# Optimization experiments

Measured on AMD Instinct MI355X. Metric: run time of the kernel, lower is better.

The kernel has to match this reference:

```python
import jax, jax.numpy as jnp
import numpy as np

N_NODES = 100000
N_EDGES = 1600000
IN_DIM = 64
OUT_DIM = 64
BN_EPS = 1e-5


def batchnorm(h, gamma, beta):
    # BatchNorm1d in training mode: per-feature batch stats, biased variance
    mean = jnp.mean(h, axis=0)
    var = jnp.mean((h - mean) ** 2, axis=0)
    return gamma * (h - mean) * jax.lax.rsqrt(var + BN_EPS) + beta


def setup_inputs() -> dict:
    key = jax.random.key(0)
    ks = jax.random.split(key, 4)
    x = jax.random.normal(ks[0], (N_NODES, IN_DIM), dtype=jnp.float32)
    edge_index = jax.random.randint(ks[1], (2, N_EDGES), 0, N_NODES, dtype=jnp.int32)
    epsilon = jnp.asarray(0.1, dtype=jnp.float32)
    # Linear weights stored [in, out] (transpose of torch layout)
    W1 = jax.random.normal(ks[2], (IN_DIM, 2 * OUT_DIM), dtype=jnp.float32) * (1.0 / np.sqrt(IN_DIM))
    b1 = jnp.zeros((2 * OUT_DIM,), dtype=jnp.float32)
    g1 = jnp.ones((2 * OUT_DIM,), dtype=jnp.float32)
    be1 = jnp.zeros((2 * OUT_DIM,), dtype=jnp.float32)
    W2 = jax.random.normal(ks[3], (2 * OUT_DIM, OUT_DIM), dtype=jnp.float32) * (1.0 / np.sqrt(2 * OUT_DIM))
    b2 = jnp.zeros((OUT_DIM,), dtype=jnp.float32)
    g2 = jnp.ones((OUT_DIM,), dtype=jnp.float32)
    be2 = jnp.zeros((OUT_DIM,), dtype=jnp.float32)
    return {"x": x, "edge_index": edge_index, "epsilon": epsilon,
            "W1": W1, "b1": b1, "g1": g1, "be1": be1,
            "W2": W2, "b2": b2, "g2": g2, "be2": be2}


def reference(x, edge_index, epsilon, W1, b1, g1, be1, W2, b2, g2, be2):
    src, dst = edge_index[0], edge_index[1]
    # gather messages from src, scatter-add into dst  [N, D]
    neighbor_sum = jnp.zeros_like(x).at[dst].add(x[src])
    combined = (1.0 + epsilon) * x + neighbor_sum
    h = combined @ W1 + b1            # [N, 2*out_dim]
    h = jax.nn.relu(batchnorm(h, g1, be1))
    h = h @ W2 + b2                   # [N, out_dim]
    return batchnorm(h, g2, be2)
```

## Files before the change

kernel.cpp:

```cpp
#include <hip/hip_runtime.h>

#define N_NODES 100000
#define N_EDGES 1600000
#define IN_DIM 64
#define H_DIM 128
#define OUT_DIM 64
#define BN_EPS 1e-5f
#define CAP 64
#define BIN_SHIFT 9
#define BIN_NODES 512
#define NB 256
#define NBIN_BLOCKS ((N_NODES + BIN_NODES - 1) / BIN_NODES)

#define OFF_XB    0
#define OFF_COMB  3200000
#define OFF_H1    6400000
#define OFF_H2    12800000
#define OFF_STATS 19200000
#define S1SUM 0
#define S1SQ  128
#define S2SUM 256
#define S2SQ  320
#define STATS_FLOATS 768

#define DEV_ATOMIC_ADD(p, v) __hip_atomic_fetch_add((p), (v), __ATOMIC_RELAXED, __HIP_MEMORY_SCOPE_AGENT)

typedef __attribute__((ext_vector_type(8))) short short8;
typedef __attribute__((ext_vector_type(4))) float f32x4;

__device__ __forceinline__ unsigned short f2bf(float f) {
  union { float f; unsigned u; } v; v.f = f;
  unsigned r = v.u + 0x7FFFu + ((v.u >> 16) & 1u);
  return (unsigned short)(r >> 16);
}
__device__ __forceinline__ float bflo(unsigned v) { union { unsigned u; float f; } t; t.u = v << 16; return t.f; }
__device__ __forceinline__ float bfhi(unsigned v) { union { unsigned u; float f; } t; t.u = v & 0xFFFF0000u; return t.f; }

__device__ __forceinline__ void acc8(float* a, uint4 v) {
  a[0] += bflo(v.x); a[1] += bfhi(v.x); a[2] += bflo(v.y); a[3] += bfhi(v.y);
  a[4] += bflo(v.z); a[5] += bfhi(v.z); a[6] += bflo(v.w); a[7] += bfhi(v.w);
}
__device__ __forceinline__ uint4 pack8(const float* a) {
  uint4 o;
  o.x = (unsigned)f2bf(a[0]) | ((unsigned)f2bf(a[1]) << 16);
  o.y = (unsigned)f2bf(a[2]) | ((unsigned)f2bf(a[3]) << 16);
  o.z = (unsigned)f2bf(a[4]) | ((unsigned)f2bf(a[5]) << 16);
  o.w = (unsigned)f2bf(a[6]) | ((unsigned)f2bf(a[7]) << 16);
  return o;
}

__global__ __launch_bounds__(256) void k_cvt(const float* __restrict__ x,
                                             unsigned short* __restrict__ xb) {
  int i = blockIdx.x * 256 + threadIdx.x;
  if (i < N_NODES * IN_DIM / 4) {
    float4 v = ((const float4*)x)[i];
    ushort4 o;
    o.x = f2bf(v.x); o.y = f2bf(v.y); o.z = f2bf(v.z); o.w = f2bf(v.w);
    *(ushort4*)(xb + i * 4) = o;
  }
}

__global__ __launch_bounds__(256) void k_bhist(const int* __restrict__ ei,
                                               int* __restrict__ bhist) {
  __shared__ int h[NB];
  const int tid = threadIdx.x;
  h[tid] = 0;
  __syncthreads();
  #pragma unroll
  for (int j = 0; j < 8; ++j) {
    int e = blockIdx.x * 2048 + j * 256 + tid;
    if (e < N_EDGES) atomicAdd(&h[ei[N_EDGES + e] >> BIN_SHIFT], 1);
  }
  __syncthreads();
  if (h[tid]) DEV_ATOMIC_ADD(&bhist[tid], h[tid]);
}

__global__ __launch_bounds__(256) void k_scan256(const int* __restrict__ bhist,
                                                 int* __restrict__ boff,
                                                 int* __restrict__ bcur) {
  __shared__ int s[NB];
  const int tid = threadIdx.x;
  int v = bhist[tid];
  s[tid] = v;
  __syncthreads();
  for (int d = 1; d < NB; d <<= 1) {
    int t = (tid >= d) ? s[tid - d] : 0;
    __syncthreads();
    s[tid] += t;
    __syncthreads();
  }
  int incl = s[tid];
  boff[tid] = incl - v;
  if (tid == NB - 1) boff[NB] = incl;
  bcur[tid] = incl - v;
}

__global__ __launch_bounds__(256) void k_bsplit(const int* __restrict__ ei,
                                                int* __restrict__ bcur,
                                                int2* __restrict__ binned) {
  __shared__ int lcnt[NB];
  __shared__ int lofs[NB];
  __shared__ int lbase[NB];
  __shared__ int sc[NB];
  __shared__ int2 staged[2048];
  const int tid = threadIdx.x;
  lcnt[tid] = 0;
  __syncthreads();
  int src[8], dst[8], rk[8];
  #pragma unroll
  for (int j = 0; j < 8; ++j) {
    int e = blockIdx.x * 2048 + j * 256 + tid;
    if (e < N_EDGES) {
      src[j] = ei[e];
      dst[j] = ei[N_EDGES + e];
      rk[j] = atomicAdd(&lcnt[dst[j] >> BIN_SHIFT], 1);
    } else {
      src[j] = -1;
    }
  }
  __syncthreads();
  int v = lcnt[tid];
  sc[tid] = v;
  __syncthreads();
  for (int d = 1; d < NB; d <<= 1) {
    int t = (tid >= d) ? sc[tid - d] : 0;
    __syncthreads();
    sc[tid] += t;
    __syncthreads();
  }
  lofs[tid] = sc[tid] - v;
  if (v > 0) lbase[tid] = DEV_ATOMIC_ADD(&bcur[tid], v);
  __syncthreads();
  #pragma unroll
  for (int j = 0; j < 8; ++j) {
    if (src[j] >= 0) {
      int b = dst[j] >> BIN_SHIFT;
      staged[lofs[b] + rk[j]] = make_int2(src[j], dst[j]);
    }
  }
  int nv = sc[NB - 1];
  __syncthreads();
  for (int i = tid; i < nv; i += 256) {
    int2 e = staged[i];
    int b = e.y >> BIN_SHIFT;
    binned[lbase[b] + (i - lofs[b])] = e;
  }
}

__global__ __launch_bounds__(512) void k_bfill(const int* __restrict__ boff,
                                               const int2* __restrict__ binned,
                                               int* __restrict__ cnt,
                                               int* __restrict__ srcl) {
  __shared__ int lcnt[BIN_NODES];
  const int tid = threadIdx.x;
  for (int i = tid; i < BIN_NODES; i += 512) lcnt[i] = 0;
  __syncthreads();
  const int b = blockIdx.x;
  const int s = boff[b], e = boff[b + 1];
  const int base = b * BIN_NODES;
  for (int i = s + tid; i < e; i += 512) {
    int2 ed = binned[i];
    int pos = atomicAdd(&lcnt[ed.y - base], 1);
    if (pos < CAP) srcl[ed.y * CAP + pos] = ed.x;
  }
  __syncthreads();
  for (int i = tid; i < BIN_NODES; i += 512) {
    int node = base + i;
    if (node < N_NODES) cnt[node] = lcnt[i];
  }
}

__global__ __launch_bounds__(256) void k_gather(const unsigned short* __restrict__ xb,
                                                const float* __restrict__ eps,
                                                const int* __restrict__ cnt,
                                                const int* __restrict__ srcl,
                                                unsigned short* __restrict__ comb) {
  int gid = blockIdx.x * 256 + threadIdx.x;
  int node = gid >> 2;
  int c = gid & 3;
  if (node >= N_NODES) return;
  float a[16];
  #pragma unroll
  for (int i = 0; i < 16; ++i) a[i] = 0.f;
  const unsigned short* bp = xb + node * 64 + c * 16;
  acc8(a, *(const uint4*)bp);
  acc8(a + 8, *(const uint4*)(bp + 8));
  float e = 1.0f + eps[0];
  #pragma unroll
  for (int i = 0; i < 16; ++i) a[i] *= e;
  int deg = cnt[node];
  if (deg > CAP) deg = CAP;
  const int* sl = srcl + node * CAP;
  int j = 0;
  for (; j + 2 <= deg; j += 2) {
    int s0 = sl[j], s1 = sl[j + 1];
    const unsigned short* p0 = xb + s0 * 64 + c * 16;
    const unsigned short* p1 = xb + s1 * 64 + c * 16;
    uint4 v0 = *(const uint4*)p0;
    uint4 v1 = *(const uint4*)(p0 + 8);
    uint4 w0 = *(const uint4*)p1;
    uint4 w1 = *(const uint4*)(p1 + 8);
    acc8(a, v0); acc8(a + 8, v1);
    acc8(a, w0); acc8(a + 8, w1);
  }
  if (j < deg) {
    const unsigned short* p0 = xb + sl[j] * 64 + c * 16;
    acc8(a, *(const uint4*)p0);
    acc8(a + 8, *(const uint4*)(p0 + 8));
  }
  unsigned short* op = comb + node * 64 + c * 16;
  *(uint4*)op = pack8(a);
  *(uint4*)(op + 8) = pack8(a + 8);
}

#define APAD 72
__global__ __launch_bounds__(256) void k_gemm1(const unsigned short* __restrict__ comb,
                                               const float* __restrict__ W1,
                                               const float* __restrict__ b1,
                                               unsigned short* __restrict__ h1,
                                               float* __restrict__ stats) {
  __shared__ unsigned short As[128 * APAD];
  __shared__ unsigned short Ws[128 * APAD];
  __shared__ float red[4][128];
  const int tid = threadIdx.x;
  const int wv = tid >> 6, lane = tid & 63;
  const int quad = lane >> 4, ln = lane & 15;
  const int rowBase = blockIdx.x * 128;

  #pragma unroll
  for (int it = 0; it < 4; ++it) {
    int idx = it * 256 + tid;
    int row = idx >> 3, ch = idx & 7;
    int gRow = rowBase + row;
    uint4 v = (gRow < N_NODES) ? *(const uint4*)(comb + gRow * 64 + ch * 8)
                               : make_uint4(0, 0, 0, 0);
    *(uint4*)&As[row * APAD + ch * 8] = v;
  }
  #pragma unroll
  for (int it = 0; it < 8; ++it) {
    int idx = it * 256 + tid;
    int k = idx >> 5, n4 = idx & 31;
    float4 wv1 = *(const float4*)(W1 + k * 128 + n4 * 4);
    Ws[(n4 * 4 + 0) * APAD + k] = f2bf(wv1.x);
    Ws[(n4 * 4 + 1) * APAD + k] = f2bf(wv1.y);
    Ws[(n4 * 4 + 2) * APAD + k] = f2bf(wv1.z);
    Ws[(n4 * 4 + 3) * APAD + k] = f2bf(wv1.w);
  }
  __syncthreads();

  f32x4 acc[2][8];
  #pragma unroll
  for (int mt = 0; mt < 2; ++mt) {
    #pragma unroll
    for (int nt = 0; nt < 8; ++nt) acc[mt][nt] = (f32x4)0.0f;
  }
  const int rw = wv * 32;
  #pragma unroll
  for (int kb = 0; kb < 2; ++kb) {
    short8 a0 = *(short8*)&As[(rw + ln) * APAD + kb * 32 + quad * 8];
    short8 a1 = *(short8*)&As[(rw + 16 + ln) * APAD + kb * 32 + quad * 8];
    #pragma unroll
    for (int nt = 0; nt < 8; ++nt) {
      short8 b = *(short8*)&Ws[(nt * 16 + ln) * APAD + kb * 32 + quad * 8];
      acc[0][nt] = __builtin_amdgcn_mfma_f32_16x16x32_bf16(a0, b, acc[0][nt], 0, 0, 0);
      acc[1][nt] = __builtin_amdgcn_mfma_f32_16x16x32_bf16(a1, b, acc[1][nt], 0, 0, 0);
    }
  }

  float bias[8], s[8], q[8];
  #pragma unroll
  for (int nt = 0; nt < 8; ++nt) { bias[nt] = b1[nt * 16 + ln]; s[nt] = 0.f; q[nt] = 0.f; }
  #pragma unroll
  for (int mt = 0; mt < 2; ++mt) {
    #pragma unroll
    for (int i = 0; i < 4; ++i) {
      int gRow = rowBase + rw + mt * 16 + quad * 4 + i;
      if (gRow < N_NODES) {
        #pragma unroll
        for (int nt = 0; nt < 8; ++nt) {
          float v = acc[mt][nt][i] + bias[nt];
          h1[gRow * 128 + nt * 16 + ln] = f2bf(v);
          s[nt] += v; q[nt] += v * v;
        }
      }
    }
  }
  #pragma unroll
  for (int nt = 0; nt < 8; ++nt) {
    s[nt] += __shfl_xor(s[nt], 16); s[nt] += __shfl_xor(s[nt], 32);
    q[nt] += __shfl_xor(q[nt], 16); q[nt] += __shfl_xor(q[nt], 32);
  }
  if (lane < 16) {
    #pragma unroll
    for (int nt = 0; nt < 8; ++nt) red[wv][nt * 16 + ln] = s[nt];
  }
  __syncthreads();
  if (tid < 128) DEV_ATOMIC_ADD(&stats[S1SUM + tid],
                                red[0][tid] + red[1][tid] + red[2][tid] + red[3][tid]);
  __syncthreads();
  if (lane < 16) {
    #pragma unroll
    for (int nt = 0; nt < 8; ++nt) red[wv][nt * 16 + ln] = q[nt];
  }
  __syncthreads();
  if (tid < 128) DEV_ATOMIC_ADD(&stats[S1SQ + tid],
                                red[0][tid] + red[1][tid] + red[2][tid] + red[3][tid]);
}

#define WPAD 136
__global__ __launch_bounds__(256) void k_gemm2(const unsigned short* __restrict__ h1,
                                               const float* __restrict__ W2,
                                               const float* __restrict__ b2,
                                               const float* __restrict__ g1,
                                               const float* __restrict__ be1,
                                               unsigned short* __restrict__ h2,
                                               float* __restrict__ stats) {
  __shared__ unsigned short As[128 * APAD];
  __shared__ unsigned short Ws[64 * WPAD];
  __shared__ float red[4][64];
  __shared__ float scL[128], shL[128];
  const int tid = threadIdx.x;
  const int wv = tid >> 6, lane = tid & 63;
  const int quad = lane >> 4, ln = lane & 15;
  const int rowBase = blockIdx.x * 128;

  if (tid < 128) {
    float mean = stats[S1SUM + tid] * (1.0f / N_NODES);
    float var = stats[S1SQ + tid] * (1.0f / N_NODES) - mean * mean;
    var = fmaxf(var, 0.0f);
    float sc = g1[tid] * rsqrtf(var + BN_EPS);
    scL[tid] = sc;
    shL[tid] = be1[tid] - mean * sc;
  }
  #pragma unroll
  for (int it = 0; it < 8; ++it) {
    int idx = it * 256 + tid;
    int k = idx >> 4, n4 = idx & 15;
    float4 wv2 = *(const float4*)(W2 + k * 64 + n4 * 4);
    Ws[(n4 * 4 + 0) * WPAD + k] = f2bf(wv2.x);
    Ws[(n4 * 4 + 1) * WPAD + k] = f2bf(wv2.y);
    Ws[(n4 * 4 + 2) * WPAD + k] = f2bf(wv2.z);
    Ws[(n4 * 4 + 3) * WPAD + k] = f2bf(wv2.w);
  }

  f32x4 acc[2][4];
  #pragma unroll
  for (int mt = 0; mt < 2; ++mt) {
    #pragma unroll
    for (int nt = 0; nt < 4; ++nt) acc[mt][nt] = (f32x4)0.0f;
  }
  const int rw = wv * 32;

  for (int kc = 0; kc < 2; ++kc) {
    __syncthreads();
    #pragma unroll
    for (int it = 0; it < 4; ++it) {
      int idx = it * 256 + tid;
      int row = idx >> 3, ch = idx & 7;
      int gRow = rowBase + row;
      uint4 u = (gRow < N_NODES) ? *(const uint4*)(h1 + gRow * 128 + kc * 64 + ch * 8)
                                 : make_uint4(0, 0, 0, 0);
      int kb = kc * 64 + ch * 8;
      float f0 = fmaxf(bflo(u.x) * scL[kb + 0] + shL[kb + 0], 0.f);
      float f1 = fmaxf(bfhi(u.x) * scL[kb + 1] + shL[kb + 1], 0.f);
      float f2 = fmaxf(bflo(u.y) * scL[kb + 2] + shL[kb + 2], 0.f);
      float f3 = fmaxf(bfhi(u.y) * scL[kb + 3] + shL[kb + 3], 0.f);
      float f4 = fmaxf(bflo(u.z) * scL[kb + 4] + shL[kb + 4], 0.f);
      float f5 = fmaxf(bfhi(u.z) * scL[kb + 5] + shL[kb + 5], 0.f);
      float f6 = fmaxf(bflo(u.w) * scL[kb + 6] + shL[kb + 6], 0.f);
      float f7 = fmaxf(bfhi(u.w) * scL[kb + 7] + shL[kb + 7], 0.f);
      uint4 o;
      o.x = (unsigned)f2bf(f0) | ((unsigned)f2bf(f1) << 16);
      o.y = (unsigned)f2bf(f2) | ((unsigned)f2bf(f3) << 16);
      o.z = (unsigned)f2bf(f4) | ((unsigned)f2bf(f5) << 16);
      o.w = (unsigned)f2bf(f6) | ((unsigned)f2bf(f7) << 16);
      *(uint4*)&As[row * APAD + ch * 8] = o;
    }
    __syncthreads();
    #pragma unroll
    for (int kb = 0; kb < 2; ++kb) {
      short8 a0 = *(short8*)&As[(rw + ln) * APAD + kb * 32 + quad * 8];
      short8 a1 = *(short8*)&As[(rw + 16 + ln) * APAD + kb * 32 + quad * 8];
      #pragma unroll
      for (int nt = 0; nt < 4; ++nt) {
        short8 b = *(short8*)&Ws[(nt * 16 + ln) * WPAD + kc * 64 + kb * 32 + quad * 8];
        acc[0][nt] = __builtin_amdgcn_mfma_f32_16x16x32_bf16(a0, b, acc[0][nt], 0, 0, 0);
        acc[1][nt] = __builtin_amdgcn_mfma_f32_16x16x32_bf16(a1, b, acc[1][nt], 0, 0, 0);
      }
    }
  }

  float bias[4], s[4], q[4];
  #pragma unroll
  for (int nt = 0; nt < 4; ++nt) { bias[nt] = b2[nt * 16 + ln]; s[nt] = 0.f; q[nt] = 0.f; }
  #pragma unroll
  for (int mt = 0; mt < 2; ++mt) {
    #pragma unroll
    for (int i = 0; i < 4; ++i) {
      int gRow = rowBase + rw + mt * 16 + quad * 4 + i;
      if (gRow < N_NODES) {
        #pragma unroll
        for (int nt = 0; nt < 4; ++nt) {
          float v = acc[mt][nt][i] + bias[nt];
          h2[gRow * 64 + nt * 16 + ln] = f2bf(v);
          s[nt] += v; q[nt] += v * v;
        }
      }
    }
  }
  #pragma unroll
  for (int nt = 0; nt < 4; ++nt) {
    s[nt] += __shfl_xor(s[nt], 16); s[nt] += __shfl_xor(s[nt], 32);
    q[nt] += __shfl_xor(q[nt], 16); q[nt] += __shfl_xor(q[nt], 32);
  }
  if (lane < 16) {
    #pragma unroll
    for (int nt = 0; nt < 4; ++nt) red[wv][nt * 16 + ln] = s[nt];
  }
  __syncthreads();
  if (tid < 64) DEV_ATOMIC_ADD(&stats[S2SUM + tid],
                               red[0][tid] + red[1][tid] + red[2][tid] + red[3][tid]);
  __syncthreads();
  if (lane < 16) {
    #pragma unroll
    for (int nt = 0; nt < 4; ++nt) red[wv][nt * 16 + ln] = q[nt];
  }
  __syncthreads();
  if (tid < 64) DEV_ATOMIC_ADD(&stats[S2SQ + tid],
                               red[0][tid] + red[1][tid] + red[2][tid] + red[3][tid]);
}

__global__ __launch_bounds__(256) void k_out(const unsigned short* __restrict__ h2,
                                             const float* __restrict__ stats,
                                             const float* __restrict__ g2,
                                             const float* __restrict__ be2,
                                             float* __restrict__ out) {
  __shared__ float scL[64], shL[64];
  const int tid = threadIdx.x;
  if (tid < 64) {
    float mean = stats[S2SUM + tid] * (1.0f / N_NODES);
    float var = stats[S2SQ + tid] * (1.0f / N_NODES) - mean * mean;
    var = fmaxf(var, 0.0f);
    float sc = g2[tid] * rsqrtf(var + BN_EPS);
    scL[tid] = sc;
    shL[tid] = be2[tid] - mean * sc;
  }
  __syncthreads();
  int i = blockIdx.x * 256 + tid;
  if (i < N_NODES * OUT_DIM / 4) {
    int c = i & 15;
    uint2 u = *(const uint2*)(h2 + i * 4);
    float4 v = {bflo(u.x), bfhi(u.x), bflo(u.y), bfhi(u.y)};
    float4 sc = ((const float4*)scL)[c];
    float4 sh = ((const float4*)shL)[c];
    v.x = v.x * sc.x + sh.x;
    v.y = v.y * sc.y + sh.y;
    v.z = v.z * sc.z + sh.z;
    v.w = v.w * sc.w + sh.w;
    ((float4*)out)[i] = v;
  }
}

extern "C" void kernel_launch(void* const* d_in, const int* in_sizes, int n_in,
                              void* d_out, int out_size, void* d_ws, size_t ws_size,
                              hipStream_t stream) {
  const float* x   = (const float*)d_in[0];
  const int*   ei  = (const int*)d_in[1];
  const float* eps = (const float*)d_in[2];
  const float* W1  = (const float*)d_in[3];
  const float* b1  = (const float*)d_in[4];
  const float* g1  = (const float*)d_in[5];
  const float* be1 = (const float*)d_in[6];
  const float* W2  = (const float*)d_in[7];
  const float* b2  = (const float*)d_in[8];
  const float* g2  = (const float*)d_in[9];
  const float* be2 = (const float*)d_in[10];

  float* ws = (float*)d_ws;
  unsigned short* xb   = (unsigned short*)(ws + OFF_XB);
  unsigned short* comb = (unsigned short*)(ws + OFF_COMB);
  int2*           binned = (int2*)(ws + OFF_COMB);
  unsigned short* h1   = (unsigned short*)(ws + OFF_H1);
  int*            srcl = (int*)(ws + OFF_H1);
  unsigned short* h2   = (unsigned short*)(ws + OFF_H2);
  int*            cnt  = (int*)(ws + OFF_H2);
  int*            bhist = cnt + N_NODES;
  int*            boff  = bhist + NB;
  int*            bcur  = boff + NB + 7;
  float*          stats = ws + OFF_STATS;
  float*          out   = (float*)d_out;

  hipMemsetAsync(stats, 0, STATS_FLOATS * sizeof(float), stream);
  hipMemsetAsync(bhist, 0, NB * sizeof(int), stream);

  const int edgeGrid = (N_EDGES + 2047) / 2048;
  const int gemmGrid = (N_NODES + 127) / 128;
  k_cvt<<<(N_NODES * IN_DIM / 4 + 255) / 256, 256, 0, stream>>>(x, xb);
  k_bhist<<<edgeGrid, 256, 0, stream>>>(ei, bhist);
  k_scan256<<<1, NB, 0, stream>>>(bhist, boff, bcur);
  k_bsplit<<<edgeGrid, 256, 0, stream>>>(ei, bcur, binned);
  k_bfill<<<NBIN_BLOCKS, 512, 0, stream>>>(boff, binned, cnt, srcl);
  k_gather<<<(N_NODES * 4 + 255) / 256, 256, 0, stream>>>(xb, eps, cnt, srcl, comb);
  k_gemm1<<<gemmGrid, 256, 0, stream>>>(comb, W1, b1, h1, stats);
  k_gemm2<<<gemmGrid, 256, 0, stream>>>(h1, W2, b2, g1, be1, h2, stats);
  k_out<<<(N_NODES * OUT_DIM / 4 + 255) / 256, 256, 0, stream>>>(h2, stats, g2, be2, out);
}
```

Measured before the change: 272.4 us.

## Fuse neighbor gather into first GEMM and merge conversion with histogram

The per-node neighbor aggregation is computed directly into the shared-memory A tile of the first GEMM, so the intermediate combined tensor is never written to or read from global memory. The bf16 conversion of x is merged into the edge histogram kernel, and the two memsets become one by moving the bin counters next to the stats buffer. Each node is now gathered by 2 threads instead of 4, which lowers memory-level parallelism and raises register use in the GEMM kernel.

Measured after the change: 254.2 us. 1.07x faster.

```diff
diff --git a/kernel.cpp b/kernel.cpp
--- a/kernel.cpp
+++ b/kernel.cpp
@@ -12,16 +12,15 @@
 #define NB 256
 #define NBIN_BLOCKS ((N_NODES + BIN_NODES - 1) / BIN_NODES)
 
-#define OFF_XB    0
-#define OFF_COMB  3200000
-#define OFF_H1    6400000
-#define OFF_H2    12800000
-#define OFF_STATS 19200000
+#define OFF_XB     0
+#define OFF_BINNED 3200000
+#define OFF_H1     6400000
+#define OFF_H2     12800000
+#define OFF_STATS  19200000
 #define S1SUM 0
 #define S1SQ  128
 #define S2SUM 256
 #define S2SQ  320
-#define STATS_FLOATS 768
 
 #define DEV_ATOMIC_ADD(p, v) __hip_atomic_fetch_add((p), (v), __ATOMIC_RELAXED, __HIP_MEMORY_SCOPE_AGENT)
 
@@ -49,22 +48,23 @@
   return o;
 }
 
-__global__ __launch_bounds__(256) void k_cvt(const float* __restrict__ x,
-                                             unsigned short* __restrict__ xb) {
-  int i = blockIdx.x * 256 + threadIdx.x;
-  if (i < N_NODES * IN_DIM / 4) {
-    float4 v = ((const float4*)x)[i];
-    ushort4 o;
-    o.x = f2bf(v.x); o.y = f2bf(v.y); o.z = f2bf(v.z); o.w = f2bf(v.w);
-    *(ushort4*)(xb + i * 4) = o;
-  }
-}
-
-__global__ __launch_bounds__(256) void k_bhist(const int* __restrict__ ei,
-                                               int* __restrict__ bhist) {
+__global__ __launch_bounds__(256) void k_prep(const float* __restrict__ x,
+                                              unsigned short* __restrict__ xb,
+                                              const int* __restrict__ ei,
+                                              int* __restrict__ bhist) {
   __shared__ int h[NB];
   const int tid = threadIdx.x;
   h[tid] = 0;
+  #pragma unroll
+  for (int j = 0; j < 8; ++j) {
+    int i = blockIdx.x * 2048 + j * 256 + tid;
+    if (i < N_NODES * IN_DIM / 4) {
+      float4 v = ((const float4*)x)[i];
+      ushort4 o;
+      o.x = f2bf(v.x); o.y = f2bf(v.y); o.z = f2bf(v.z); o.w = f2bf(v.w);
+      *(ushort4*)(xb + i * 4) = o;
+    }
+  }
   __syncthreads();
   #pragma unroll
   for (int j = 0; j < 8; ++j) {
@@ -170,51 +170,11 @@
   }
 }
 
-__global__ __launch_bounds__(256) void k_gather(const unsigned short* __restrict__ xb,
-                                                const float* __restrict__ eps,
-                                                const int* __restrict__ cnt,
-                                                const int* __restrict__ srcl,
-                                                unsigned short* __restrict__ comb) {
-  int gid = blockIdx.x * 256 + threadIdx.x;
-  int node = gid >> 2;
-  int c = gid & 3;
-  if (node >= N_NODES) return;
-  float a[16];
-  #pragma unroll
-  for (int i = 0; i < 16; ++i) a[i] = 0.f;
-  const unsigned short* bp = xb + node * 64 + c * 16;
-  acc8(a, *(const uint4*)bp);
-  acc8(a + 8, *(const uint4*)(bp + 8));
-  float e = 1.0f + eps[0];
-  #pragma unroll
-  for (int i = 0; i < 16; ++i) a[i] *= e;
-  int deg = cnt[node];
-  if (deg > CAP) deg = CAP;
-  const int* sl = srcl + node * CAP;
-  int j = 0;
-  for (; j + 2 <= deg; j += 2) {
-    int s0 = sl[j], s1 = sl[j + 1];
-    const unsigned short* p0 = xb + s0 * 64 + c * 16;
-    const unsigned short* p1 = xb + s1 * 64 + c * 16;
-    uint4 v0 = *(const uint4*)p0;
-    uint4 v1 = *(const uint4*)(p0 + 8);
-    uint4 w0 = *(const uint4*)p1;
-    uint4 w1 = *(const uint4*)(p1 + 8);
-    acc8(a, v0); acc8(a + 8, v1);
-    acc8(a, w0); acc8(a + 8, w1);
-  }
-  if (j < deg) {
-    const unsigned short* p0 = xb + sl[j] * 64 + c * 16;
-    acc8(a, *(const uint4*)p0);
-    acc8(a + 8, *(const uint4*)(p0 + 8));
-  }
-  unsigned short* op = comb + node * 64 + c * 16;
-  *(uint4*)op = pack8(a);
-  *(uint4*)(op + 8) = pack8(a + 8);
-}
-
 #define APAD 72
-__global__ __launch_bounds__(256) void k_gemm1(const unsigned short* __restrict__ comb,
+__global__ __launch_bounds__(256) void k_fuse1(const unsigned short* __restrict__ xb,
+                                               const float* __restrict__ eps,
+                                               const int* __restrict__ cnt,
+                                               const int* __restrict__ srcl,
                                                const float* __restrict__ W1,
                                                const float* __restrict__ b1,
                                                unsigned short* __restrict__ h1,
@@ -227,15 +187,6 @@
   const int quad = lane >> 4, ln = lane & 15;
   const int rowBase = blockIdx.x * 128;
 
-  #pragma unroll
-  for (int it = 0; it < 4; ++it) {
-    int idx = it * 256 + tid;
-    int row = idx >> 3, ch = idx & 7;
-    int gRow = rowBase + row;
-    uint4 v = (gRow < N_NODES) ? *(const uint4*)(comb + gRow * 64 + ch * 8)
-                               : make_uint4(0, 0, 0, 0);
-    *(uint4*)&As[row * APAD + ch * 8] = v;
-  }
   #pragma unroll
   for (int it = 0; it < 8; ++it) {
     int idx = it * 256 + tid;
@@ -245,6 +196,55 @@
     Ws[(n4 * 4 + 1) * APAD + k] = f2bf(wv1.y);
     Ws[(n4 * 4 + 2) * APAD + k] = f2bf(wv1.z);
     Ws[(n4 * 4 + 3) * APAD + k] = f2bf(wv1.w);
+  }
+
+  {
+    int row = tid >> 1;
+    int half = tid & 1;
+    int node = rowBase + row;
+    float a[32];
+    #pragma unroll
+    for (int i = 0; i < 32; ++i) a[i] = 0.f;
+    if (node < N_NODES) {
+      const unsigned short* bp = xb + node * 64 + half * 32;
+      acc8(a, *(const uint4*)bp);
+      acc8(a + 8, *(const uint4*)(bp + 8));
+      acc8(a + 16, *(const uint4*)(bp + 16));
+      acc8(a + 24, *(const uint4*)(bp + 24));
+      float e = 1.0f + eps[0];
+      #pragma unroll
+      for (int i = 0; i < 32; ++i) a[i] *= e;
+      int deg = cnt[node];
+      if (deg > CAP) deg = CAP;
+      const int* sl = srcl + node * CAP;
+      int j = 0;
+      for (; j + 2 <= deg; j += 2) {
+        const unsigned short* p0 = xb + sl[j] * 64 + half * 32;
+        const unsigned short* p1 = xb + sl[j + 1] * 64 + half * 32;
+        uint4 v0 = *(const uint4*)p0;
+        uint4 v1 = *(const uint4*)(p0 + 8);
+        uint4 v2 = *(const uint4*)(p0 + 16);
+        uint4 v3 = *(const uint4*)(p0 + 24);
+        uint4 w0 = *(const uint4*)p1;
+        uint4 w1 = *(const uint4*)(p1 + 8);
+        uint4 w2 = *(const uint4*)(p1 + 16);
+        uint4 w3 = *(const uint4*)(p1 + 24);
+        acc8(a, v0); acc8(a + 8, v1); acc8(a + 16, v2); acc8(a + 24, v3);
+        acc8(a, w0); acc8(a + 8, w1); acc8(a + 16, w2); acc8(a + 24, w3);
+      }
+      if (j < deg) {
+        const unsigned short* p0 = xb + sl[j] * 64 + half * 32;
+        acc8(a, *(const uint4*)p0);
+        acc8(a + 8, *(const uint4*)(p0 + 8));
+        acc8(a + 16, *(const uint4*)(p0 + 16));
+        acc8(a + 24, *(const uint4*)(p0 + 24));
+      }
+    }
+    unsigned short* ap = &As[row * APAD + half * 32];
+    *(uint4*)ap = pack8(a);
+    *(uint4*)(ap + 8) = pack8(a + 8);
+    *(uint4*)(ap + 16) = pack8(a + 16);
+    *(uint4*)(ap + 24) = pack8(a + 24);
   }
   __syncthreads();
 
@@ -477,31 +477,27 @@
   const float* be2 = (const float*)d_in[10];
 
   float* ws = (float*)d_ws;
-  unsigned short* xb   = (unsigned short*)(ws + OFF_XB);
-  unsigned short* comb = (unsigned short*)(ws + OFF_COMB);
-  int2*           binned = (int2*)(ws + OFF_COMB);
-  unsigned short* h1   = (unsigned short*)(ws + OFF_H1);
-  int*            srcl = (int*)(ws + OFF_H1);
-  unsigned short* h2   = (unsigned short*)(ws + OFF_H2);
-  int*            cnt  = (int*)(ws + OFF_H2);
-  int*            bhist = cnt + N_NODES;
-  int*            boff  = bhist + NB;
-  int*            bcur  = boff + NB + 7;
-  float*          stats = ws + OFF_STATS;
-  float*          out   = (float*)d_out;
-
-  hipMemsetAsync(stats, 0, STATS_FLOATS * sizeof(float), stream);
-  hipMemsetAsync(bhist, 0, NB * sizeof(int), stream);
+  unsigned short* xb     = (unsigned short*)(ws + OFF_XB);
+  int2*           binned = (int2*)(ws + OFF_BINNED);
+  unsigned short* h1     = (unsigned short*)(ws + OFF_H1);
+  int*            srcl   = (int*)(ws + OFF_H1);
+  unsigned short* h2     = (unsigned short*)(ws + OFF_H2);
+  int*            cnt    = (int*)(ws + OFF_H2);
+  float*          stats  = ws + OFF_STATS;
+  int*            bhist  = (int*)(stats + 768);
+  int*            boff   = (int*)(stats + 1024);
+  int*            bcur   = (int*)(stats + 1288);
+  float*          out    = (float*)d_out;
+
+  hipMemsetAsync(stats, 0, 1024 * sizeof(float), stream);
 
   const int edgeGrid = (N_EDGES + 2047) / 2048;
   const int gemmGrid = (N_NODES + 127) / 128;
-  k_cvt<<<(N_NODES * IN_DIM / 4 + 255) / 256, 256, 0, stream>>>(x, xb);
-  k_bhist<<<edgeGrid, 256, 0, stream>>>(ei, bhist);
+  k_prep<<<edgeGrid, 256, 0, stream>>>(x, xb, ei, bhist);
   k_scan256<<<1, NB, 0, stream>>>(bhist, boff, bcur);
   k_bsplit<<<edgeGrid, 256, 0, stream>>>(ei, bcur, binned);
   k_bfill<<<NBIN_BLOCKS, 512, 0, stream>>>(boff, binned, cnt, srcl);
-  k_gather<<<(N_NODES * 4 + 255) / 256, 256, 0, stream>>>(xb, eps, cnt, srcl, comb);
-  k_gemm1<<<gemmGrid, 256, 0, stream>>>(comb, W1, b1, h1, stats);
+  k_fuse1<<<gemmGrid, 256, 0, stream>>>(xb, eps, cnt, srcl, W1, b1, h1, stats);
   k_gemm2<<<gemmGrid, 256, 0, stream>>>(h1, W2, b2, g1, be1, h2, stats);
   k_out<<<(N_NODES * OUT_DIM / 4 + 255) / 256, 256, 0, stream>>>(h2, stats, g2, be2, out);
 }
```
